# Kernel tuning notes

Hardware: AMD Instinct MI355X
Metric: run time of the kernel (lower is better)

## Reference

```python
import jax, jax.numpy as jnp
import numpy as np

D_MODEL = 1024
NUM_HEADS = 16
D_K = D_MODEL // NUM_HEADS
B, S = 2, 2048


def setup_inputs() -> dict:
    key = jax.random.key(0)
    ks = jax.random.split(key, 12)
    scale = 1.0 / np.sqrt(D_MODEL)
    inp = {
        "q": jax.random.normal(ks[0], (B, S, D_MODEL), jnp.float32),
        "k": jax.random.normal(ks[1], (B, S, D_MODEL), jnp.float32),
        "v": jax.random.normal(ks[2], (B, S, D_MODEL), jnp.float32),
        # causal mask: True means "mask out" (masked_fill semantics)
        "mask": jnp.triu(jnp.ones((S, S), jnp.bool_), k=1)[None, None, :, :],
        "w_q": jax.random.normal(ks[3], (D_MODEL, D_MODEL), jnp.float32) * scale,
        "b_q": jax.random.normal(ks[4], (D_MODEL,), jnp.float32) * scale,
        "w_k": jax.random.normal(ks[5], (D_MODEL, D_MODEL), jnp.float32) * scale,
        "b_k": jax.random.normal(ks[6], (D_MODEL,), jnp.float32) * scale,
        "w_v": jax.random.normal(ks[7], (D_MODEL, D_MODEL), jnp.float32) * scale,
        "b_v": jax.random.normal(ks[8], (D_MODEL,), jnp.float32) * scale,
        "w_o": jax.random.normal(ks[9], (D_MODEL, D_MODEL), jnp.float32) * scale,
        "b_o": jax.random.normal(ks[10], (D_MODEL,), jnp.float32) * scale,
    }
    return inp


def reference(q, k, v, mask, w_q, b_q, w_k, b_k, w_v, b_v, w_o, b_o):
    Bq, S_, _ = q.shape
    # torch Linear: x @ W.T + b
    queries = q @ w_q.T + b_q
    keys = k @ w_k.T + b_k
    values = v @ w_v.T + b_v
    # (B, S, H, Dk) -> (B, H, S, Dk)
    queries = queries.reshape(Bq, S_, NUM_HEADS, D_K).transpose(0, 2, 1, 3)
    keys = keys.reshape(Bq, S_, NUM_HEADS, D_K).transpose(0, 2, 1, 3)
    values = values.reshape(Bq, S_, NUM_HEADS, D_K).transpose(0, 2, 1, 3)
    scores = jnp.einsum("bhqd,bhkd->bhqk", queries, keys) / jnp.sqrt(
        jnp.asarray(D_K, queries.dtype)
    )
    scores = jnp.where(mask, -jnp.inf, scores)
    attn = jax.nn.softmax(scores, axis=-1)
    out = jnp.einsum("bhqk,bhkd->bhqd", attn, values)
    out = out.transpose(0, 2, 1, 3).reshape(Bq, S_, D_MODEL)
    out = out @ w_o.T + b_o
    return out, attn
```

## Files before the change

kernel.cpp:

```cpp
#include <hip/hip_runtime.h>
#include <hip/hip_bf16.h>
#include <math.h>

#define S_LEN 2048
#define NH 16
#define DK 64
#define DM 1024
#define BB 2
#define NROWS (BB * S_LEN)
#define BHN (BB * NH)

typedef __attribute__((ext_vector_type(8))) short short8;
typedef __attribute__((ext_vector_type(8))) unsigned short u16x8;
typedef __attribute__((ext_vector_type(4))) float f32x4;

#define LDS_W 72

#define AS1C(p) ((const __attribute__((address_space(1))) void*)(p))
#define AS3(p)  ((__attribute__((address_space(3))) void*)(p))

__device__ __forceinline__ unsigned short f2bf(float x) {
  return __builtin_bit_cast(unsigned short, __float2bfloat16(x));
}
__device__ __forceinline__ float bf2f(unsigned short u) {
  return __uint_as_float(((unsigned)u) << 16);
}

struct ConvArgs {
  const float* src[8];
  unsigned short* dst[8];
  int n8[8];
};

__global__ __launch_bounds__(256)
void convert_all(ConvArgs a) {
  const int t = blockIdx.y;
  const float* __restrict__ s = a.src[t];
  unsigned short* __restrict__ d = a.dst[t];
  const int n8 = a.n8[t];
  for (int idx = blockIdx.x * 256 + threadIdx.x; idx < n8; idx += gridDim.x * 256) {
    const long f = (long)idx * 8;
    const float4 x0 = *(const float4*)(s + f);
    const float4 x1 = *(const float4*)(s + f + 4);
    const float xs[8] = {x0.x, x0.y, x0.z, x0.w, x1.x, x1.y, x1.z, x1.w};
    u16x8 hv, lv;
    #pragma unroll
    for (int j = 0; j < 8; ++j) {
      const unsigned short h = f2bf(xs[j]);
      hv[j] = h;
      lv[j] = f2bf(xs[j] - bf2f(h));
    }
    const long chunk = f >> 5;
    const int pos = (int)(f & 31);
    unsigned short* base = d + (chunk << 6) + pos;
    *(u16x8*)(base) = hv;
    *(u16x8*)(base + 32) = lv;
  }
}

template<int MODE>
__global__ __launch_bounds__(256)
void plane_gemm(const unsigned short* __restrict__ Ap,
                const unsigned short* __restrict__ Bp,
                const float* __restrict__ bias, float* __restrict__ C)
{
  __shared__ unsigned short sA[2][128 * 128];
  __shared__ unsigned short sB[2][128 * 128];
  const int tid = threadIdx.x;
  const int lane = tid & 63, w = tid >> 6;
  const int wr = w >> 1, wc = w & 1;
  const int lr = lane & 15, lg = lane >> 4;
  const int m0 = blockIdx.y * 128, n0 = blockIdx.x * 128;

  const unsigned short* gsrc = (w < 2) ? Ap : Bp;
  const int rowbase = ((w < 2) ? m0 : n0) + (w & 1) * 64;
  const int sl = lane & 15;
  const int rl = lane >> 4;
  const int cb = sl >> 3;
  const int s7 = sl & 7;

  f32x4 acc[4][4];
  #pragma unroll
  for (int m = 0; m < 4; ++m)
    #pragma unroll
    for (int n = 0; n < 4; ++n) acc[m][n] = (f32x4){0.f, 0.f, 0.f, 0.f};

  auto stage = [&](int kt, int buf) {
    unsigned short* lbase = ((w < 2) ? sA[buf] : sB[buf]) + (w & 1) * 8192;
    #pragma unroll
    for (int i = 0; i < 16; ++i) {
      const int r = i * 4 + rl;
      const size_t grow = (size_t)(rowbase + r);
      const size_t so = grow * 2048 + (size_t)(kt * 2 + cb) * 64 + ((s7 ^ (r & 7)) * 8);
      __builtin_amdgcn_global_load_lds(AS1C(gsrc + so), AS3(lbase + i * 512), 16, 0, 0);
    }
  };

  stage(0, 0);
  __syncthreads();
  int buf = 0;
  for (int kt = 0; kt < 16; ++kt) {
    #pragma unroll
    for (int kk = 0; kk < 2; ++kk) {
      short8 ah[4], al[4], bh[4], bl[4];
      #pragma unroll
      for (int m = 0; m < 4; ++m) {
        const int rr = wr * 64 + m * 16 + lr;
        const unsigned short* base = sA[buf] + rr * 128 + kk * 64;
        ah[m] = *(const short8*)(base + ((lg       ^ (rr & 7)) * 8));
        al[m] = *(const short8*)(base + (((lg + 4) ^ (rr & 7)) * 8));
      }
      #pragma unroll
      for (int n = 0; n < 4; ++n) {
        const int rr = wc * 64 + n * 16 + lr;
        const unsigned short* base = sB[buf] + rr * 128 + kk * 64;
        bh[n] = *(const short8*)(base + ((lg       ^ (rr & 7)) * 8));
        bl[n] = *(const short8*)(base + (((lg + 4) ^ (rr & 7)) * 8));
      }
      if (kk == 0 && kt < 15) stage(kt + 1, buf ^ 1);
      #pragma unroll
      for (int m = 0; m < 4; ++m)
        #pragma unroll
        for (int n = 0; n < 4; ++n) {
          acc[m][n] = __builtin_amdgcn_mfma_f32_16x16x32_bf16(ah[m], bh[n], acc[m][n], 0, 0, 0);
          acc[m][n] = __builtin_amdgcn_mfma_f32_16x16x32_bf16(al[m], bh[n], acc[m][n], 0, 0, 0);
          acc[m][n] = __builtin_amdgcn_mfma_f32_16x16x32_bf16(ah[m], bl[n], acc[m][n], 0, 0, 0);
        }
    }
    __syncthreads();
    buf ^= 1;
  }

  #pragma unroll
  for (int n = 0; n < 4; ++n) {
    const int col = n0 + wc * 64 + n * 16 + lr;
    const float bb = bias[col];
    #pragma unroll
    for (int m = 0; m < 4; ++m) {
      const int rbase = m0 + wr * 64 + m * 16 + lg * 4;
      #pragma unroll
      for (int j = 0; j < 4; ++j) {
        const int row = rbase + j;
        const float o = acc[m][n][j] + bb;
        if (MODE == 0) {
          C[(size_t)row * DM + col] = o;
        } else {
          const int b = row >> 11, s = row & (S_LEN - 1);
          const int h = col >> 6, d = col & 63;
          C[(((size_t)(b * NH + h) * S_LEN + s) * DK + d)] = o;
        }
      }
    }
  }
}

__device__ __forceinline__ void stage128x64(const float* __restrict__ base, int ld,
                                            unsigned short* sh, unsigned short* sl,
                                            int tid) {
  #pragma unroll
  for (int i = 0; i < 4; ++i) {
    const int f = tid + i * 256;
    const int r = f >> 3;
    const int c = (f & 7) * 8;
    const float* p = base + (size_t)r * ld + c;
    const float4 v0 = *(const float4*)(p);
    const float4 v1 = *(const float4*)(p + 4);
    const float xs[8] = {v0.x, v0.y, v0.z, v0.w, v1.x, v1.y, v1.z, v1.w};
    u16x8 hv, lv;
    #pragma unroll
    for (int j = 0; j < 8; ++j) {
      const unsigned short h = f2bf(xs[j]);
      hv[j] = h;
      lv[j] = f2bf(xs[j] - bf2f(h));
    }
    *(u16x8*)(sh + r * LDS_W + c) = hv;
    *(u16x8*)(sl + r * LDS_W + c) = lv;
  }
}

__global__ __launch_bounds__(256)
void scores_kernel(const float* __restrict__ Qp, const float* __restrict__ Kp,
                   float* __restrict__ attn)
{
  __shared__ unsigned short As_h[128 * LDS_W], As_l[128 * LDS_W];
  __shared__ unsigned short Bs_h[128 * LDS_W], Bs_l[128 * LDS_W];
  const int tid = threadIdx.x;
  const int lane = tid & 63, wv = tid >> 6;
  const int wr = wv >> 1, wc = wv & 1;
  const int lr = lane & 15, lg = lane >> 4;
  const int r = blockIdx.x;
  int qb = 0;
  while ((qb + 1) * (qb + 2) / 2 <= r) qb++;
  const int kb = r - qb * (qb + 1) / 2;
  const int m0 = qb * 128, n0 = kb * 128;
  const float* Ab = Qp + ((size_t)blockIdx.y * S_LEN + m0) * DK;
  const float* Bb = Kp + ((size_t)blockIdx.y * S_LEN + n0) * DK;

  f32x4 acc[4][4];
  #pragma unroll
  for (int m = 0; m < 4; ++m)
    #pragma unroll
    for (int n = 0; n < 4; ++n) acc[m][n] = (f32x4){0.f, 0.f, 0.f, 0.f};

  stage128x64(Ab, DK, As_h, As_l, tid);
  stage128x64(Bb, DK, Bs_h, Bs_l, tid);
  __syncthreads();
  #pragma unroll
  for (int kk = 0; kk < 2; ++kk) {
    short8 ah[4], al[4], bh2[4], bl2[4];
    #pragma unroll
    for (int m = 0; m < 4; ++m) {
      const int off = (wr * 64 + m * 16 + lr) * LDS_W + kk * 32 + lg * 8;
      ah[m] = *(const short8*)(As_h + off);
      al[m] = *(const short8*)(As_l + off);
    }
    #pragma unroll
    for (int n = 0; n < 4; ++n) {
      const int off = (wc * 64 + n * 16 + lr) * LDS_W + kk * 32 + lg * 8;
      bh2[n] = *(const short8*)(Bs_h + off);
      bl2[n] = *(const short8*)(Bs_l + off);
    }
    #pragma unroll
    for (int m = 0; m < 4; ++m)
      #pragma unroll
      for (int n = 0; n < 4; ++n) {
        acc[m][n] = __builtin_amdgcn_mfma_f32_16x16x32_bf16(ah[m], bh2[n], acc[m][n], 0, 0, 0);
        acc[m][n] = __builtin_amdgcn_mfma_f32_16x16x32_bf16(al[m], bh2[n], acc[m][n], 0, 0, 0);
        acc[m][n] = __builtin_amdgcn_mfma_f32_16x16x32_bf16(ah[m], bl2[n], acc[m][n], 0, 0, 0);
      }
  }

  #pragma unroll
  for (int n = 0; n < 4; ++n) {
    const int col = n0 + wc * 64 + n * 16 + lr;
    #pragma unroll
    for (int m = 0; m < 4; ++m) {
      const int rbase = m0 + wr * 64 + m * 16 + lg * 4;
      #pragma unroll
      for (int j = 0; j < 4; ++j) {
        attn[((size_t)blockIdx.y * S_LEN + rbase + j) * S_LEN + col] = acc[m][n][j] * 0.125f;
      }
    }
  }
}

__global__ __launch_bounds__(256)
void softmax_kernel(float* __restrict__ attn)
{
  const int row = blockIdx.x;
  const int q = row & (S_LEN - 1);
  float* rowp = attn + (size_t)row * S_LEN;
  const int t = threadIdx.x;

  float vals[8];
  float m = -INFINITY;
  #pragma unroll
  for (int i = 0; i < 2; ++i) {
    const int c0 = (i * 256 + t) * 4;
    float4 x = make_float4(-INFINITY, -INFINITY, -INFINITY, -INFINITY);
    if (c0 <= q) x = *(const float4*)(rowp + c0);
    vals[i * 4 + 0] = (c0 + 0 <= q) ? x.x : -INFINITY;
    vals[i * 4 + 1] = (c0 + 1 <= q) ? x.y : -INFINITY;
    vals[i * 4 + 2] = (c0 + 2 <= q) ? x.z : -INFINITY;
    vals[i * 4 + 3] = (c0 + 3 <= q) ? x.w : -INFINITY;
    m = fmaxf(m, fmaxf(fmaxf(vals[i*4], vals[i*4+1]), fmaxf(vals[i*4+2], vals[i*4+3])));
  }
  #pragma unroll
  for (int off = 32; off > 0; off >>= 1)
    m = fmaxf(m, __shfl_xor(m, off));
  __shared__ float red[8];
  if ((t & 63) == 0) red[t >> 6] = m;
  __syncthreads();
  m = fmaxf(fmaxf(red[0], red[1]), fmaxf(red[2], red[3]));

  float s = 0.f;
  #pragma unroll
  for (int i = 0; i < 8; ++i) {
    const float e = __expf(vals[i] - m);
    vals[i] = e;
    s += e;
  }
  #pragma unroll
  for (int off = 32; off > 0; off >>= 1)
    s += __shfl_xor(s, off);
  if ((t & 63) == 0) red[4 + (t >> 6)] = s;
  __syncthreads();
  s = (red[4] + red[5]) + (red[6] + red[7]);
  const float inv = 1.0f / s;

  #pragma unroll
  for (int i = 0; i < 2; ++i) {
    const int c0 = (i * 256 + t) * 4;
    float4 o;
    o.x = vals[i * 4 + 0] * inv;
    o.y = vals[i * 4 + 1] * inv;
    o.z = vals[i * 4 + 2] * inv;
    o.w = vals[i * 4 + 3] * inv;
    *(float4*)(rowp + c0) = o;
  }
}

__global__ __launch_bounds__(256)
void pv_mfma(const float* __restrict__ attn, const float* __restrict__ Vp,
             float* __restrict__ ctx)
{
  __shared__ unsigned short As_h[128 * LDS_W], As_l[128 * LDS_W];
  __shared__ unsigned short Vs_h[64 * LDS_W],  Vs_l[64 * LDS_W];
  const int tid = threadIdx.x;
  const int lane = tid & 63, wv = tid >> 6;
  const int lr = lane & 15, lg = lane >> 4;
  const int bh = blockIdx.y;
  const int qb = 15 - blockIdx.x;
  const int q0 = qb * 128;
  const float* Ab = attn + ((size_t)bh * S_LEN + q0) * S_LEN;
  const float* Vb = Vp + (size_t)bh * S_LEN * DK;

  f32x4 acc[2][4];
  #pragma unroll
  for (int m = 0; m < 2; ++m)
    #pragma unroll
    for (int n = 0; n < 4; ++n) acc[m][n] = (f32x4){0.f, 0.f, 0.f, 0.f};

  const int nk = (q0 + 128) / 64;
  for (int kt = 0; kt < nk; ++kt) {
    stage128x64(Ab + kt * 64, S_LEN, As_h, As_l, tid);
    #pragma unroll
    for (int i = 0; i < 4; ++i) {
      const int g = tid + i * 256;
      const int kr = g >> 4;
      const int c4 = (g & 15) * 4;
      const float4 v = *(const float4*)(Vb + (size_t)(kt * 64 + kr) * DK + c4);
      const float xs[4] = {v.x, v.y, v.z, v.w};
      #pragma unroll
      for (int j = 0; j < 4; ++j) {
        const unsigned short h = f2bf(xs[j]);
        Vs_h[(c4 + j) * LDS_W + kr] = h;
        Vs_l[(c4 + j) * LDS_W + kr] = f2bf(xs[j] - bf2f(h));
      }
    }
    __syncthreads();
    #pragma unroll
    for (int kk = 0; kk < 2; ++kk) {
      short8 ah[2], al[2], bh2[4], bl2[4];
      #pragma unroll
      for (int m = 0; m < 2; ++m) {
        const int off = (wv * 32 + m * 16 + lr) * LDS_W + kk * 32 + lg * 8;
        ah[m] = *(const short8*)(As_h + off);
        al[m] = *(const short8*)(As_l + off);
      }
      #pragma unroll
      for (int n = 0; n < 4; ++n) {
        const int off = (n * 16 + lr) * LDS_W + kk * 32 + lg * 8;
        bh2[n] = *(const short8*)(Vs_h + off);
        bl2[n] = *(const short8*)(Vs_l + off);
      }
      #pragma unroll
      for (int m = 0; m < 2; ++m)
        #pragma unroll
        for (int n = 0; n < 4; ++n) {
          acc[m][n] = __builtin_amdgcn_mfma_f32_16x16x32_bf16(ah[m], bh2[n], acc[m][n], 0, 0, 0);
          acc[m][n] = __builtin_amdgcn_mfma_f32_16x16x32_bf16(al[m], bh2[n], acc[m][n], 0, 0, 0);
          acc[m][n] = __builtin_amdgcn_mfma_f32_16x16x32_bf16(ah[m], bl2[n], acc[m][n], 0, 0, 0);
        }
    }
    __syncthreads();
  }

  const int b = bh >> 4, h = bh & 15;
  #pragma unroll
  for (int n = 0; n < 4; ++n) {
    const int d = n * 16 + lr;
    #pragma unroll
    for (int m = 0; m < 2; ++m) {
      #pragma unroll
      for (int j = 0; j < 4; ++j) {
        const int s = q0 + wv * 32 + m * 16 + lg * 4 + j;
        ctx[((size_t)b * S_LEN + s) * DM + h * DK + d] = acc[m][n][j];
      }
    }
  }
}

extern "C" void kernel_launch(void* const* d_in, const int* in_sizes, int n_in,
                              void* d_out, int out_size, void* d_ws, size_t ws_size,
                              hipStream_t stream) {
  const float* q   = (const float*)d_in[0];
  const float* k   = (const float*)d_in[1];
  const float* v   = (const float*)d_in[2];
  const float* w_q = (const float*)d_in[4];
  const float* b_q = (const float*)d_in[5];
  const float* w_k = (const float*)d_in[6];
  const float* b_k = (const float*)d_in[7];
  const float* w_v = (const float*)d_in[8];
  const float* b_v = (const float*)d_in[9];
  const float* w_o = (const float*)d_in[10];
  const float* b_o = (const float*)d_in[11];

  float* out  = (float*)d_out;
  float* attn = out + (size_t)NROWS * DM;

  const size_t MB = 1024 * 1024;
  char* wsb = (char*)d_ws;
  unsigned short* qP  = (unsigned short*)(wsb + 0 * MB);
  unsigned short* kP  = (unsigned short*)(wsb + 16 * MB);
  unsigned short* vP  = (unsigned short*)(wsb + 32 * MB);
  unsigned short* wqP = (unsigned short*)(wsb + 48 * MB);
  unsigned short* wkP = (unsigned short*)(wsb + 52 * MB);
  unsigned short* wvP = (unsigned short*)(wsb + 56 * MB);
  unsigned short* woP = (unsigned short*)(wsb + 60 * MB);
  float* Qp  = (float*)(wsb + 64 * MB);
  float* Kp  = (float*)(wsb + 80 * MB);
  float* Vp  = (float*)(wsb + 96 * MB);
  float* ctx = (float*)(wsb + 112 * MB);
  unsigned short* cP = (unsigned short*)(wsb + 128 * MB);

  ConvArgs ca = {};
  ca.src[0] = q;   ca.dst[0] = qP;  ca.n8[0] = NROWS * DM / 8;
  ca.src[1] = k;   ca.dst[1] = kP;  ca.n8[1] = NROWS * DM / 8;
  ca.src[2] = v;   ca.dst[2] = vP;  ca.n8[2] = NROWS * DM / 8;
  ca.src[3] = w_q; ca.dst[3] = wqP; ca.n8[3] = DM * DM / 8;
  ca.src[4] = w_k; ca.dst[4] = wkP; ca.n8[4] = DM * DM / 8;
  ca.src[5] = w_v; ca.dst[5] = wvP; ca.n8[5] = DM * DM / 8;
  ca.src[6] = w_o; ca.dst[6] = woP; ca.n8[6] = DM * DM / 8;
  ca.src[7] = q;   ca.dst[7] = qP;  ca.n8[7] = 0;
  convert_all<<<dim3(2048, 7), 256, 0, stream>>>(ca);

  const dim3 gproj(DM / 128, NROWS / 128);
  plane_gemm<1><<<gproj, 256, 0, stream>>>(qP, wqP, b_q, Qp);
  plane_gemm<1><<<gproj, 256, 0, stream>>>(kP, wkP, b_k, Kp);
  plane_gemm<1><<<gproj, 256, 0, stream>>>(vP, wvP, b_v, Vp);

  scores_kernel<<<dim3(136, BHN), 256, 0, stream>>>(Qp, Kp, attn);
  softmax_kernel<<<dim3(BB * NH * S_LEN), 256, 0, stream>>>(attn);
  pv_mfma<<<dim3(16, BHN), 256, 0, stream>>>(attn, Vp, ctx);

  ConvArgs cc = {};
  cc.src[0] = ctx; cc.dst[0] = cP; cc.n8[0] = NROWS * DM / 8;
  for (int i = 1; i < 8; ++i) { cc.src[i] = ctx; cc.dst[i] = cP; cc.n8[i] = 0; }
  convert_all<<<dim3(2048, 1), 256, 0, stream>>>(cc);
  plane_gemm<0><<<gproj, 256, 0, stream>>>(cP, woP, b_o, out);
}
```

Baseline: 1.053 ms.

## Fuse scores, softmax and PV into a two-pass flash-style attention kernel

Replaces the separate scores, softmax and PV kernels with one fused kernel. A first pass over the K tiles computes the running row max and sum; a second pass recomputes the scores, writes the normalized attention probabilities once, and multiplies them by V held in LDS. Q, K and transposed V are pre-split into bf16 hi/lo planes with XOR-swizzled layouts and loaded with direct global-to-LDS copies. A separate kernel zeroes the masked upper triangle of the attention output. This removes the round trips of the attention matrix through global memory between kernels, in exchange for computing QK^T twice and adding extra conversion kernels.

```diff
diff --git a/kernel.cpp b/kernel.cpp
--- a/kernel.cpp
+++ b/kernel.cpp
@@ -14,10 +14,9 @@
 typedef __attribute__((ext_vector_type(8))) unsigned short u16x8;
 typedef __attribute__((ext_vector_type(4))) float f32x4;
 
-#define LDS_W 72
-
 #define AS1C(p) ((const __attribute__((address_space(1))) void*)(p))
 #define AS3(p)  ((__attribute__((address_space(3))) void*)(p))
+#define SW(s, r) ((s) ^ ((r) & 7))
 
 __device__ __forceinline__ unsigned short f2bf(float x) {
   return __builtin_bit_cast(unsigned short, __float2bfloat16(x));
@@ -56,6 +55,79 @@
     *(u16x8*)(base) = hv;
     *(u16x8*)(base + 32) = lv;
   }
+}
+
+__global__ __launch_bounds__(256)
+void conv_qk(const float* __restrict__ src, unsigned short* __restrict__ dst, int n8) {
+  for (int idx = blockIdx.x * 256 + threadIdx.x; idx < n8; idx += gridDim.x * 256) {
+    const long g = (long)idx * 8;
+    const int row = (int)(g >> 6);
+    const int k0 = (int)(g & 63);
+    const float4 x0 = *(const float4*)(src + g);
+    const float4 x1 = *(const float4*)(src + g + 4);
+    const float xs[8] = {x0.x, x0.y, x0.z, x0.w, x1.x, x1.y, x1.z, x1.w};
+    u16x8 hv, lv;
+    #pragma unroll
+    for (int j = 0; j < 8; ++j) {
+      const unsigned short h = f2bf(xs[j]);
+      hv[j] = h;
+      lv[j] = f2bf(xs[j] - bf2f(h));
+    }
+    const int c = k0 >> 5, sq = (k0 & 31) >> 3;
+    const int s0 = c * 8 + sq;
+    unsigned short* base = dst + (size_t)row * 128;
+    *(u16x8*)(base + SW(s0, row) * 8) = hv;
+    *(u16x8*)(base + SW(s0 + 4, row) * 8) = lv;
+  }
+}
+
+__global__ __launch_bounds__(256)
+void conv_vt(const float* __restrict__ Vp, unsigned short* __restrict__ Vt) {
+  __shared__ float T[64][65];
+  const int kblk = blockIdx.x, bh = blockIdx.y;
+  const int tid = threadIdx.x;
+  const float* src = Vp + ((size_t)bh * S_LEN + kblk * 64) * DK;
+  #pragma unroll
+  for (int i = 0; i < 4; ++i) {
+    const int idx = tid + i * 256;
+    const int kr = idx >> 4, dc = (idx & 15) * 4;
+    const float4 v = *(const float4*)(src + (size_t)kr * DK + dc);
+    T[kr][dc] = v.x; T[kr][dc + 1] = v.y; T[kr][dc + 2] = v.z; T[kr][dc + 3] = v.w;
+  }
+  __syncthreads();
+  unsigned short* dtile = Vt + (size_t)(bh * 32 + kblk) * 64 * 128;
+  #pragma unroll
+  for (int i = 0; i < 2; ++i) {
+    const int u = tid + i * 256;
+    const int d = u >> 3, ko = (u & 7) * 8;
+    float xs[8];
+    #pragma unroll
+    for (int j = 0; j < 8; ++j) xs[j] = T[ko + j][d];
+    u16x8 hv, lv;
+    #pragma unroll
+    for (int j = 0; j < 8; ++j) {
+      const unsigned short h = f2bf(xs[j]);
+      hv[j] = h;
+      lv[j] = f2bf(xs[j] - bf2f(h));
+    }
+    const int c = ko >> 5, sq = (ko & 31) >> 3;
+    const int s0 = c * 8 + sq;
+    unsigned short* base = dtile + d * 128;
+    *(u16x8*)(base + SW(s0, d) * 8) = hv;
+    *(u16x8*)(base + SW(s0 + 4, d) * 8) = lv;
+  }
+}
+
+__global__ __launch_bounds__(256)
+void zero_upper(float* __restrict__ attn) {
+  const int qt = blockIdx.x;
+  const int bh = blockIdx.y;
+  const int c0 = (qt + 1) * 64;
+  float* base = attn + ((size_t)bh * S_LEN + qt * 64) * S_LEN;
+  const float4 z = {0.f, 0.f, 0.f, 0.f};
+  for (int r = 0; r < 64; ++r)
+    for (int c = c0 + threadIdx.x * 4; c < S_LEN; c += 1024)
+      *(float4*)(base + (size_t)r * S_LEN + c) = z;
 }
 
 template<int MODE>
@@ -154,231 +226,241 @@
   }
 }
 
-__device__ __forceinline__ void stage128x64(const float* __restrict__ base, int ld,
-                                            unsigned short* sh, unsigned short* sl,
-                                            int tid) {
-  #pragma unroll
-  for (int i = 0; i < 4; ++i) {
-    const int f = tid + i * 256;
-    const int r = f >> 3;
-    const int c = (f & 7) * 8;
-    const float* p = base + (size_t)r * ld + c;
-    const float4 v0 = *(const float4*)(p);
-    const float4 v1 = *(const float4*)(p + 4);
-    const float xs[8] = {v0.x, v0.y, v0.z, v0.w, v1.x, v1.y, v1.z, v1.w};
-    u16x8 hv, lv;
-    #pragma unroll
-    for (int j = 0; j < 8; ++j) {
-      const unsigned short h = f2bf(xs[j]);
-      hv[j] = h;
-      lv[j] = f2bf(xs[j] - bf2f(h));
-    }
-    *(u16x8*)(sh + r * LDS_W + c) = hv;
-    *(u16x8*)(sl + r * LDS_W + c) = lv;
-  }
-}
-
-__global__ __launch_bounds__(256)
-void scores_kernel(const float* __restrict__ Qp, const float* __restrict__ Kp,
-                   float* __restrict__ attn)
+__global__ __launch_bounds__(256, 2)
+void fused_attn(const unsigned short* __restrict__ Qpl,
+                const unsigned short* __restrict__ Kpl,
+                const unsigned short* __restrict__ Vtpl,
+                float* __restrict__ attn, float* __restrict__ ctx)
 {
-  __shared__ unsigned short As_h[128 * LDS_W], As_l[128 * LDS_W];
-  __shared__ unsigned short Bs_h[128 * LDS_W], Bs_l[128 * LDS_W];
+  __shared__ unsigned short Ks[2][64 * 128];
+  __shared__ unsigned short Vs[64 * 128];
+  __shared__ unsigned short PQs[64 * 128];
+  __shared__ float m_l[64], l_l[64], redm[2][64], reds[2][64];
+
   const int tid = threadIdx.x;
-  const int lane = tid & 63, wv = tid >> 6;
-  const int wr = wv >> 1, wc = wv & 1;
+  const int lane = tid & 63, w = tid >> 6;
+  const int wr = w >> 1, wc = w & 1;
   const int lr = lane & 15, lg = lane >> 4;
-  const int r = blockIdx.x;
-  int qb = 0;
-  while ((qb + 1) * (qb + 2) / 2 <= r) qb++;
-  const int kb = r - qb * (qb + 1) / 2;
-  const int m0 = qb * 128, n0 = kb * 128;
-  const float* Ab = Qp + ((size_t)blockIdx.y * S_LEN + m0) * DK;
-  const float* Bb = Kp + ((size_t)blockIdx.y * S_LEN + n0) * DK;
-
-  f32x4 acc[4][4];
-  #pragma unroll
-  for (int m = 0; m < 4; ++m)
-    #pragma unroll
-    for (int n = 0; n < 4; ++n) acc[m][n] = (f32x4){0.f, 0.f, 0.f, 0.f};
-
-  stage128x64(Ab, DK, As_h, As_l, tid);
-  stage128x64(Bb, DK, Bs_h, Bs_l, tid);
+
+  const int wg = blockIdx.x;
+  const int xcd = wg & 7, ii = wg >> 3;
+  const int bh = xcd * 4 + (ii & 3);
+  const int qt = 31 - (ii >> 2);
+  const int q0 = qt * 64;
+  const int nk = qt + 1;
+
+  const unsigned short* Qb = Qpl + ((size_t)bh * S_LEN + q0) * 128;
+  const unsigned short* Kb = Kpl + (size_t)bh * S_LEN * 128;
+  const unsigned short* Vb = Vtpl + (size_t)bh * 32 * 64 * 128;
+
+  auto stage64 = [&](const unsigned short* srcRow0, unsigned short* dst) {
+    #pragma unroll
+    for (int j = 0; j < 4; ++j) {
+      const int rb = w * 16 + j * 4;
+      const unsigned short* src = srcRow0 + (size_t)(rb + (lane >> 4)) * 128 + (lane & 15) * 8;
+      __builtin_amdgcn_global_load_lds(AS1C(src), AS3(dst + rb * 128), 16, 0, 0);
+    }
+  };
+
+  stage64(Qb, PQs);
+  stage64(Kb, Ks[0]);
+  if (tid < 64) { m_l[tid] = -INFINITY; l_l[tid] = 0.f; }
   __syncthreads();
-  #pragma unroll
-  for (int kk = 0; kk < 2; ++kk) {
-    short8 ah[4], al[4], bh2[4], bl2[4];
-    #pragma unroll
-    for (int m = 0; m < 4; ++m) {
-      const int off = (wr * 64 + m * 16 + lr) * LDS_W + kk * 32 + lg * 8;
-      ah[m] = *(const short8*)(As_h + off);
-      al[m] = *(const short8*)(As_l + off);
-    }
-    #pragma unroll
-    for (int n = 0; n < 4; ++n) {
-      const int off = (wc * 64 + n * 16 + lr) * LDS_W + kk * 32 + lg * 8;
-      bh2[n] = *(const short8*)(Bs_h + off);
-      bl2[n] = *(const short8*)(Bs_l + off);
-    }
-    #pragma unroll
-    for (int m = 0; m < 4; ++m)
-      #pragma unroll
-      for (int n = 0; n < 4; ++n) {
-        acc[m][n] = __builtin_amdgcn_mfma_f32_16x16x32_bf16(ah[m], bh2[n], acc[m][n], 0, 0, 0);
-        acc[m][n] = __builtin_amdgcn_mfma_f32_16x16x32_bf16(al[m], bh2[n], acc[m][n], 0, 0, 0);
-        acc[m][n] = __builtin_amdgcn_mfma_f32_16x16x32_bf16(ah[m], bl2[n], acc[m][n], 0, 0, 0);
-      }
-  }
-
-  #pragma unroll
-  for (int n = 0; n < 4; ++n) {
-    const int col = n0 + wc * 64 + n * 16 + lr;
-    #pragma unroll
-    for (int m = 0; m < 4; ++m) {
-      const int rbase = m0 + wr * 64 + m * 16 + lg * 4;
+
+  short8 qh[2][2], ql[2][2];
+  #pragma unroll
+  for (int mf = 0; mf < 2; ++mf) {
+    const int row = wr * 32 + mf * 16 + lr;
+    const unsigned short* base = PQs + row * 128;
+    #pragma unroll
+    for (int kk = 0; kk < 2; ++kk) {
+      qh[mf][kk] = *(const short8*)(base + SW(kk * 8 + lg, row) * 8);
+      ql[mf][kk] = *(const short8*)(base + SW(kk * 8 + 4 + lg, row) * 8);
+    }
+  }
+
+  f32x4 sacc[2][2];
+  auto compute_S = [&](const unsigned short* K, int kt) {
+    #pragma unroll
+    for (int mf = 0; mf < 2; ++mf)
+      #pragma unroll
+      for (int nf = 0; nf < 2; ++nf) sacc[mf][nf] = (f32x4){0.f, 0.f, 0.f, 0.f};
+    #pragma unroll
+    for (int kk = 0; kk < 2; ++kk) {
+      short8 kh[2], kl[2];
+      #pragma unroll
+      for (int nf = 0; nf < 2; ++nf) {
+        const int krow = wc * 32 + nf * 16 + lr;
+        const unsigned short* base = K + krow * 128;
+        kh[nf] = *(const short8*)(base + SW(kk * 8 + lg, krow) * 8);
+        kl[nf] = *(const short8*)(base + SW(kk * 8 + 4 + lg, krow) * 8);
+      }
+      #pragma unroll
+      for (int mf = 0; mf < 2; ++mf)
+        #pragma unroll
+        for (int nf = 0; nf < 2; ++nf) {
+          sacc[mf][nf] = __builtin_amdgcn_mfma_f32_16x16x32_bf16(qh[mf][kk], kh[nf], sacc[mf][nf], 0, 0, 0);
+          sacc[mf][nf] = __builtin_amdgcn_mfma_f32_16x16x32_bf16(ql[mf][kk], kh[nf], sacc[mf][nf], 0, 0, 0);
+          sacc[mf][nf] = __builtin_amdgcn_mfma_f32_16x16x32_bf16(qh[mf][kk], kl[nf], sacc[mf][nf], 0, 0, 0);
+        }
+    }
+    #pragma unroll
+    for (int mf = 0; mf < 2; ++mf)
+      #pragma unroll
+      for (int nf = 0; nf < 2; ++nf)
+        #pragma unroll
+        for (int j = 0; j < 4; ++j) {
+          float v = sacc[mf][nf][j] * 0.125f;
+          if (kt == qt) {
+            const int lcol = wc * 32 + nf * 16 + lr;
+            const int lrow = wr * 32 + mf * 16 + lg * 4 + j;
+            if (lcol > lrow) v = -INFINITY;
+          }
+          sacc[mf][nf][j] = v;
+        }
+  };
+
+  int buf = 0;
+  for (int kt = 0; kt < nk; ++kt) {
+    stage64(Kb + (size_t)((kt + 1 < nk) ? (kt + 1) : 0) * 64 * 128, Ks[buf ^ 1]);
+    compute_S(Ks[buf], kt);
+
+    float pm[2][4];
+    #pragma unroll
+    for (int mf = 0; mf < 2; ++mf)
       #pragma unroll
       for (int j = 0; j < 4; ++j) {
-        attn[((size_t)blockIdx.y * S_LEN + rbase + j) * S_LEN + col] = acc[m][n][j] * 0.125f;
-      }
-    }
-  }
-}
-
-__global__ __launch_bounds__(256)
-void softmax_kernel(float* __restrict__ attn)
-{
-  const int row = blockIdx.x;
-  const int q = row & (S_LEN - 1);
-  float* rowp = attn + (size_t)row * S_LEN;
-  const int t = threadIdx.x;
-
-  float vals[8];
-  float m = -INFINITY;
-  #pragma unroll
-  for (int i = 0; i < 2; ++i) {
-    const int c0 = (i * 256 + t) * 4;
-    float4 x = make_float4(-INFINITY, -INFINITY, -INFINITY, -INFINITY);
-    if (c0 <= q) x = *(const float4*)(rowp + c0);
-    vals[i * 4 + 0] = (c0 + 0 <= q) ? x.x : -INFINITY;
-    vals[i * 4 + 1] = (c0 + 1 <= q) ? x.y : -INFINITY;
-    vals[i * 4 + 2] = (c0 + 2 <= q) ? x.z : -INFINITY;
-    vals[i * 4 + 3] = (c0 + 3 <= q) ? x.w : -INFINITY;
-    m = fmaxf(m, fmaxf(fmaxf(vals[i*4], vals[i*4+1]), fmaxf(vals[i*4+2], vals[i*4+3])));
-  }
-  #pragma unroll
-  for (int off = 32; off > 0; off >>= 1)
-    m = fmaxf(m, __shfl_xor(m, off));
-  __shared__ float red[8];
-  if ((t & 63) == 0) red[t >> 6] = m;
-  __syncthreads();
-  m = fmaxf(fmaxf(red[0], red[1]), fmaxf(red[2], red[3]));
-
-  float s = 0.f;
-  #pragma unroll
-  for (int i = 0; i < 8; ++i) {
-    const float e = __expf(vals[i] - m);
-    vals[i] = e;
-    s += e;
-  }
-  #pragma unroll
-  for (int off = 32; off > 0; off >>= 1)
-    s += __shfl_xor(s, off);
-  if ((t & 63) == 0) red[4 + (t >> 6)] = s;
-  __syncthreads();
-  s = (red[4] + red[5]) + (red[6] + red[7]);
-  const float inv = 1.0f / s;
-
-  #pragma unroll
-  for (int i = 0; i < 2; ++i) {
-    const int c0 = (i * 256 + t) * 4;
-    float4 o;
-    o.x = vals[i * 4 + 0] * inv;
-    o.y = vals[i * 4 + 1] * inv;
-    o.z = vals[i * 4 + 2] * inv;
-    o.w = vals[i * 4 + 3] * inv;
-    *(float4*)(rowp + c0) = o;
-  }
-}
-
-__global__ __launch_bounds__(256)
-void pv_mfma(const float* __restrict__ attn, const float* __restrict__ Vp,
-             float* __restrict__ ctx)
-{
-  __shared__ unsigned short As_h[128 * LDS_W], As_l[128 * LDS_W];
-  __shared__ unsigned short Vs_h[64 * LDS_W],  Vs_l[64 * LDS_W];
-  const int tid = threadIdx.x;
-  const int lane = tid & 63, wv = tid >> 6;
-  const int lr = lane & 15, lg = lane >> 4;
-  const int bh = blockIdx.y;
-  const int qb = 15 - blockIdx.x;
-  const int q0 = qb * 128;
-  const float* Ab = attn + ((size_t)bh * S_LEN + q0) * S_LEN;
-  const float* Vb = Vp + (size_t)bh * S_LEN * DK;
-
-  f32x4 acc[2][4];
-  #pragma unroll
-  for (int m = 0; m < 2; ++m)
-    #pragma unroll
-    for (int n = 0; n < 4; ++n) acc[m][n] = (f32x4){0.f, 0.f, 0.f, 0.f};
-
-  const int nk = (q0 + 128) / 64;
+        float v = fmaxf(sacc[mf][0][j], sacc[mf][1][j]);
+        #pragma unroll
+        for (int off = 1; off < 16; off <<= 1) v = fmaxf(v, __shfl_xor(v, off));
+        pm[mf][j] = v;
+      }
+    if (lr == 0) {
+      #pragma unroll
+      for (int mf = 0; mf < 2; ++mf)
+        #pragma unroll
+        for (int j = 0; j < 4; ++j)
+          redm[wc][wr * 32 + mf * 16 + lg * 4 + j] = pm[mf][j];
+    }
+    __syncthreads();
+
+    float nm_[2][4], mo_[2][4], es_[2][4];
+    #pragma unroll
+    for (int mf = 0; mf < 2; ++mf)
+      #pragma unroll
+      for (int j = 0; j < 4; ++j) {
+        const int row = wr * 32 + mf * 16 + lg * 4 + j;
+        const float tm = fmaxf(redm[0][row], redm[1][row]);
+        mo_[mf][j] = m_l[row];
+        nm_[mf][j] = fmaxf(mo_[mf][j], tm);
+        float e = __expf(sacc[mf][0][j] - nm_[mf][j]) + __expf(sacc[mf][1][j] - nm_[mf][j]);
+        #pragma unroll
+        for (int off = 1; off < 16; off <<= 1) e += __shfl_xor(e, off);
+        es_[mf][j] = e;
+      }
+    if (lr == 0) {
+      #pragma unroll
+      for (int mf = 0; mf < 2; ++mf)
+        #pragma unroll
+        for (int j = 0; j < 4; ++j)
+          reds[wc][wr * 32 + mf * 16 + lg * 4 + j] = es_[mf][j];
+    }
+    __syncthreads();
+    if (wc == 0 && lr == 0) {
+      #pragma unroll
+      for (int mf = 0; mf < 2; ++mf)
+        #pragma unroll
+        for (int j = 0; j < 4; ++j) {
+          const int row = wr * 32 + mf * 16 + lg * 4 + j;
+          l_l[row] = l_l[row] * __expf(mo_[mf][j] - nm_[mf][j]) + reds[0][row] + reds[1][row];
+          m_l[row] = nm_[mf][j];
+        }
+    }
+    __syncthreads();
+    buf ^= 1;
+  }
+
+  float rm[2][4], rinv[2][4];
+  #pragma unroll
+  for (int mf = 0; mf < 2; ++mf)
+    #pragma unroll
+    for (int j = 0; j < 4; ++j) {
+      const int row = wr * 32 + mf * 16 + lg * 4 + j;
+      rm[mf][j] = m_l[row];
+      rinv[mf][j] = 1.0f / l_l[row];
+    }
+
+  f32x4 acc_o[2][2];
+  #pragma unroll
+  for (int mf = 0; mf < 2; ++mf)
+    #pragma unroll
+    for (int nf = 0; nf < 2; ++nf) acc_o[mf][nf] = (f32x4){0.f, 0.f, 0.f, 0.f};
+
   for (int kt = 0; kt < nk; ++kt) {
-    stage128x64(Ab + kt * 64, S_LEN, As_h, As_l, tid);
-    #pragma unroll
-    for (int i = 0; i < 4; ++i) {
-      const int g = tid + i * 256;
-      const int kr = g >> 4;
-      const int c4 = (g & 15) * 4;
-      const float4 v = *(const float4*)(Vb + (size_t)(kt * 64 + kr) * DK + c4);
-      const float xs[4] = {v.x, v.y, v.z, v.w};
+    stage64(Vb + (size_t)kt * 64 * 128, Vs);
+    if (kt + 1 < nk) stage64(Kb + (size_t)(kt + 1) * 64 * 128, Ks[buf ^ 1]);
+    compute_S(Ks[buf], kt);
+
+    #pragma unroll
+    for (int mf = 0; mf < 2; ++mf)
+      #pragma unroll
+      for (int nf = 0; nf < 2; ++nf)
+        #pragma unroll
+        for (int j = 0; j < 4; ++j) {
+          const int lrow = wr * 32 + mf * 16 + lg * 4 + j;
+          const int lcol = wc * 32 + nf * 16 + lr;
+          const float p = __expf(sacc[mf][nf][j] - rm[mf][j]) * rinv[mf][j];
+          attn[((size_t)bh * S_LEN + q0 + lrow) * S_LEN + kt * 64 + lcol] = p;
+          const unsigned short h = f2bf(p);
+          const unsigned short lo = f2bf(p - bf2f(h));
+          const int u = ((lcol >> 5) << 6) + (lcol & 31);
+          const int s0 = u >> 3, pos = u & 7;
+          PQs[lrow * 128 + SW(s0, lrow) * 8 + pos] = h;
+          PQs[lrow * 128 + SW(s0 + 4, lrow) * 8 + pos] = lo;
+        }
+    __syncthreads();
+
+    #pragma unroll
+    for (int kk = 0; kk < 2; ++kk) {
+      short8 ph[2], pl[2], vh[2], vl[2];
+      #pragma unroll
+      for (int mf = 0; mf < 2; ++mf) {
+        const int row = wr * 32 + mf * 16 + lr;
+        const unsigned short* base = PQs + row * 128;
+        ph[mf] = *(const short8*)(base + SW(kk * 8 + lg, row) * 8);
+        pl[mf] = *(const short8*)(base + SW(kk * 8 + 4 + lg, row) * 8);
+      }
+      #pragma unroll
+      for (int nf = 0; nf < 2; ++nf) {
+        const int d = wc * 32 + nf * 16 + lr;
+        const unsigned short* base = Vs + d * 128;
+        vh[nf] = *(const short8*)(base + SW(kk * 8 + lg, d) * 8);
+        vl[nf] = *(const short8*)(base + SW(kk * 8 + 4 + lg, d) * 8);
+      }
+      #pragma unroll
+      for (int mf = 0; mf < 2; ++mf)
+        #pragma unroll
+        for (int nf = 0; nf < 2; ++nf) {
+          acc_o[mf][nf] = __builtin_amdgcn_mfma_f32_16x16x32_bf16(ph[mf], vh[nf], acc_o[mf][nf], 0, 0, 0);
+          acc_o[mf][nf] = __builtin_amdgcn_mfma_f32_16x16x32_bf16(pl[mf], vh[nf], acc_o[mf][nf], 0, 0, 0);
+          acc_o[mf][nf] = __builtin_amdgcn_mfma_f32_16x16x32_bf16(ph[mf], vl[nf], acc_o[mf][nf], 0, 0, 0);
+        }
+    }
+    __syncthreads();
+    buf ^= 1;
+  }
+
+  const int b = bh >> 4, h = bh & 15;
+  #pragma unroll
+  for (int mf = 0; mf < 2; ++mf)
+    #pragma unroll
+    for (int nf = 0; nf < 2; ++nf)
       #pragma unroll
       for (int j = 0; j < 4; ++j) {
-        const unsigned short h = f2bf(xs[j]);
-        Vs_h[(c4 + j) * LDS_W + kr] = h;
-        Vs_l[(c4 + j) * LDS_W + kr] = f2bf(xs[j] - bf2f(h));
-      }
-    }
-    __syncthreads();
-    #pragma unroll
-    for (int kk = 0; kk < 2; ++kk) {
-      short8 ah[2], al[2], bh2[4], bl2[4];
-      #pragma unroll
-      for (int m = 0; m < 2; ++m) {
-        const int off = (wv * 32 + m * 16 + lr) * LDS_W + kk * 32 + lg * 8;
-        ah[m] = *(const short8*)(As_h + off);
-        al[m] = *(const short8*)(As_l + off);
-      }
-      #pragma unroll
-      for (int n = 0; n < 4; ++n) {
-        const int off = (n * 16 + lr) * LDS_W + kk * 32 + lg * 8;
-        bh2[n] = *(const short8*)(Vs_h + off);
-        bl2[n] = *(const short8*)(Vs_l + off);
-      }
-      #pragma unroll
-      for (int m = 0; m < 2; ++m)
-        #pragma unroll
-        for (int n = 0; n < 4; ++n) {
-          acc[m][n] = __builtin_amdgcn_mfma_f32_16x16x32_bf16(ah[m], bh2[n], acc[m][n], 0, 0, 0);
-          acc[m][n] = __builtin_amdgcn_mfma_f32_16x16x32_bf16(al[m], bh2[n], acc[m][n], 0, 0, 0);
-          acc[m][n] = __builtin_amdgcn_mfma_f32_16x16x32_bf16(ah[m], bl2[n], acc[m][n], 0, 0, 0);
-        }
-    }
-    __syncthreads();
-  }
-
-  const int b = bh >> 4, h = bh & 15;
-  #pragma unroll
-  for (int n = 0; n < 4; ++n) {
-    const int d = n * 16 + lr;
-    #pragma unroll
-    for (int m = 0; m < 2; ++m) {
-      #pragma unroll
-      for (int j = 0; j < 4; ++j) {
-        const int s = q0 + wv * 32 + m * 16 + lg * 4 + j;
-        ctx[((size_t)b * S_LEN + s) * DM + h * DK + d] = acc[m][n][j];
-      }
-    }
-  }
+        const int s = q0 + wr * 32 + mf * 16 + lg * 4 + j;
+        const int d = wc * 32 + nf * 16 + lr;
+        ctx[((size_t)b * S_LEN + s) * DM + h * DK + d] = acc_o[mf][nf][j];
+      }
 }
 
 extern "C" void kernel_launch(void* const* d_in, const int* in_sizes, int n_in,
@@ -401,18 +483,21 @@
 
   const size_t MB = 1024 * 1024;
   char* wsb = (char*)d_ws;
-  unsigned short* qP  = (unsigned short*)(wsb + 0 * MB);
-  unsigned short* kP  = (unsigned short*)(wsb + 16 * MB);
-  unsigned short* vP  = (unsigned short*)(wsb + 32 * MB);
-  unsigned short* wqP = (unsigned short*)(wsb + 48 * MB);
-  unsigned short* wkP = (unsigned short*)(wsb + 52 * MB);
-  unsigned short* wvP = (unsigned short*)(wsb + 56 * MB);
-  unsigned short* woP = (unsigned short*)(wsb + 60 * MB);
+  unsigned short* qP   = (unsigned short*)(wsb + 0 * MB);
+  unsigned short* kP   = (unsigned short*)(wsb + 16 * MB);
+  unsigned short* vP   = (unsigned short*)(wsb + 32 * MB);
+  unsigned short* wqP  = (unsigned short*)(wsb + 48 * MB);
+  unsigned short* wkP  = (unsigned short*)(wsb + 52 * MB);
+  unsigned short* wvP  = (unsigned short*)(wsb + 56 * MB);
+  unsigned short* woP  = (unsigned short*)(wsb + 60 * MB);
   float* Qp  = (float*)(wsb + 64 * MB);
   float* Kp  = (float*)(wsb + 80 * MB);
   float* Vp  = (float*)(wsb + 96 * MB);
   float* ctx = (float*)(wsb + 112 * MB);
-  unsigned short* cP = (unsigned short*)(wsb + 128 * MB);
+  unsigned short* cP   = (unsigned short*)(wsb + 128 * MB);
+  unsigned short* Qpl  = (unsigned short*)(wsb + 144 * MB);
+  unsigned short* Kpl  = (unsigned short*)(wsb + 160 * MB);
+  unsigned short* Vtpl = (unsigned short*)(wsb + 176 * MB);
 
   ConvArgs ca = {};
   ca.src[0] = q;   ca.dst[0] = qP;  ca.n8[0] = NROWS * DM / 8;
@@ -430,9 +515,13 @@
   plane_gemm<1><<<gproj, 256, 0, stream>>>(kP, wkP, b_k, Kp);
   plane_gemm<1><<<gproj, 256, 0, stream>>>(vP, wvP, b_v, Vp);
 
-  scores_kernel<<<dim3(136, BHN), 256, 0, stream>>>(Qp, Kp, attn);
-  softmax_kernel<<<dim3(BB * NH * S_LEN), 256, 0, stream>>>(attn);
-  pv_mfma<<<dim3(16, BHN), 256, 0, stream>>>(attn, Vp, ctx);
+  const int nqk8 = BHN * S_LEN * DK / 8;
+  conv_qk<<<2048, 256, 0, stream>>>(Qp, Qpl, nqk8);
+  conv_qk<<<2048, 256, 0, stream>>>(Kp, Kpl, nqk8);
+  conv_vt<<<dim3(32, BHN), 256, 0, stream>>>(Vp, Vtpl);
+  zero_upper<<<dim3(31, BHN), 256, 0, stream>>>(attn);
+
+  fused_attn<<<dim3(1024), 256, 0, stream>>>(Qpl, Kpl, Vtpl, attn, ctx);
 
   ConvArgs cc = {};
   cc.src[0] = ctx; cc.dst[0] = cP; cc.n8[0] = NROWS * DM / 8;
```

Result: faster. 938.6 us (-10.9%).
